# Performance work log

Measured on AMD Instinct MI355X. Metric: run time of the kernel, lower is better.

Reference implementation:

```python
import jax, jax.numpy as jnp
import numpy as np

NUM_HEADS = 16
NUM_KV_HEADS = 4
HEAD_SIZE = 128
SCALE = 1.0 / np.sqrt(128.0).astype(np.float32)
NEG_INF = -1e30


def setup_inputs() -> dict:
    key = jax.random.key(0)
    kq, kk, kv = jax.random.split(key, 3)
    B, S = 2, 2048
    query = jax.random.normal(kq, (B, NUM_HEADS, S, HEAD_SIZE), dtype=jnp.float32)
    k = jax.random.normal(kk, (B, NUM_KV_HEADS, S, HEAD_SIZE), dtype=jnp.float32)
    v = jax.random.normal(kv, (B, NUM_KV_HEADS, S, HEAD_SIZE), dtype=jnp.float32)
    return {"query": query, "key": k, "value": v}


def _attn(query, key, value):
    # query: [B, H, S, D]; key/value: [B, Hkv, S, D]; GQA with group = H // Hkv
    B, H, S, D = query.shape
    Hkv = key.shape[1]
    G = H // Hkv
    q = query.reshape(B, Hkv, G, S, D)
    # scores: [B, Hkv, G, Sq, Sk]
    scores = jnp.einsum('bkgsd,bktd->bkgst', q, key) * jnp.float32(SCALE)
    causal = jnp.tril(jnp.ones((S, S), dtype=bool))  # [Sq, Sk]
    scores = jnp.where(causal, scores, jnp.float32(NEG_INF))
    probs = jax.nn.softmax(scores, axis=-1)
    out = jnp.einsum('bkgst,bktd->bkgsd', probs, value)  # [B, Hkv, G, S, D]
    out = out.reshape(B, H, S, D)
    # transpose(1,2).reshape -> [B, S, H*D]
    return out.transpose(0, 2, 1, 3).reshape(B, S, H * D)


def reference(query, key, value):
    return _attn(query, key, value)
```

## Files before the change

kernel.cpp:

```cpp
#include <hip/hip_runtime.h>


#define S_LEN 2048
#define DH    128
#define NH    16
#define NKVH  4
#define NB    2
#define TQ    128
#define TK    64
#define NQT   (S_LEN / TQ)
#define QSCALE 0.12752749610559243f

typedef __attribute__((ext_vector_type(8))) short short8;
typedef __attribute__((ext_vector_type(4))) float f32x4;

#if __has_builtin(__builtin_amdgcn_exp2f)
#define EX2(x) __builtin_amdgcn_exp2f(x)
#else
#define EX2(x) exp2f(x)
#endif

__device__ __forceinline__ unsigned pk2(float a, float b) {
    union { float f; unsigned u; } x, y; x.f = a; y.f = b;
    return ((x.u + 0x8000u) >> 16) | ((y.u + 0x8000u) & 0xffff0000u);
}
__device__ __forceinline__ void cp16(const void* g, void* lds) {
    __builtin_amdgcn_global_load_lds(
        (const __attribute__((address_space(1))) void*)g,
        (__attribute__((address_space(3))) void*)lds, 16, 0, 0);
}

__global__ __launch_bounds__(256, 4)
void prepack(const float* __restrict__ K, const float* __restrict__ V,
             unsigned short* __restrict__ Kb, unsigned short* __restrict__ Vt) {
    if (blockIdx.y == 0) {
        const long long flat = (long long)blockIdx.x * 2048 + threadIdx.x * 8;
        const int s = (int)(flat >> 7) & (S_LEN - 1);
        const int d0 = (int)flat & 127;
        const float* p = K + flat;
        float4 x = *(const float4*)p;
        float4 y = *(const float4*)(p + 4);
        const int cs = (d0 >> 3) ^ (s & 7);
        uint4 o;
        o.x = pk2(x.x, x.y); o.y = pk2(x.z, x.w);
        o.z = pk2(y.x, y.y); o.w = pk2(y.z, y.w);
        *(uint4*)(Kb + (flat & ~127LL) + cs * 8) = o;
    } else {
        const int x = blockIdx.x;
        const int bkvh = x >> 7, sblk = (x >> 2) & 31, q = x & 3;
        const int tid = threadIdx.x;
        __shared__ unsigned Lt[64][17];
        const float* base = V + (size_t)bkvh * S_LEN * DH + (size_t)sblk * 64 * DH + q * 32;
#pragma unroll
        for (int j = 0; j < 2; ++j) {
            const int e = tid + j * 256;
            const int s = e >> 3, c4 = e & 7;
            float4 v = *(const float4*)(base + (size_t)s * DH + c4 * 4);
            Lt[s][c4 * 2]     = pk2(v.x, v.y);
            Lt[s][c4 * 2 + 1] = pk2(v.z, v.w);
        }
        __syncthreads();
        const unsigned short* lt = (const unsigned short*)&Lt[0][0];
        const int d_loc = tid >> 3, pc = tid & 7;
        const int d = q * 32 + d_loc;
        const int c_log = pc ^ (d & 7);
        unsigned short vv[8];
#pragma unroll
        for (int j = 0; j < 8; ++j) {
            const int kp = c_log * 8 + j;
            const int kv = (kp & 3) * 16 + (kp >> 2);
            vv[j] = lt[kv * 34 + d_loc];
        }
        uint4 o;
        o.x = (unsigned)vv[0] | ((unsigned)vv[1] << 16);
        o.y = (unsigned)vv[2] | ((unsigned)vv[3] << 16);
        o.z = (unsigned)vv[4] | ((unsigned)vv[5] << 16);
        o.w = (unsigned)vv[6] | ((unsigned)vv[7] << 16);
        *(uint4*)(Vt + (size_t)bkvh * S_LEN * DH + (size_t)d * S_LEN + sblk * 64 + pc * 8) = o;
    }
}

__global__ __launch_bounds__(256, 2)
void attn_fwd(const float* __restrict__ Q,
              const unsigned short* __restrict__ Kb,
              const unsigned short* __restrict__ Vtg,
              float* __restrict__ O,
              float* __restrict__ Opart,
              float* __restrict__ Lpart) {
    const int n    = blockIdx.x;
    const int g    = n & 7;
    const int b    = g >> 2;
    const int kvh  = g & 3;
    const int kk   = n >> 3;
    const int h    = kvh * 4 + (kk & 3);
    const int pr   = kk >> 2;
    const int a    = pr & 7;
    const int role = pr >> 3;
    const int sid  = ((b * NH + h) << 3) + a;

    const int tid  = threadIdx.x;
    const int w    = tid >> 6;
    const int lane = tid & 63;
    const int quad = lane >> 4;
    const int l16  = lane & 15;
    const int swz  = l16 & 7;

    int qt0, kt00, nr0, qt1; bool two_seg;
    if (role == 0) { qt0 = a;      kt00 = 0;         nr0 = 2 * a + 2;
                     qt1 = 15 - a; two_seg = true; }
    else           { qt0 = 15 - a; kt00 = 15 - 2*a;  nr0 = 17;
                     qt1 = 0;      two_seg = false; }

    __shared__ alignas(16) unsigned short Kl[2][TK][DH];
    __shared__ alignas(16) unsigned short Vl[2][DH][TK];
    __shared__ alignas(16) unsigned short Pl[TQ][64];

    const unsigned short* kb = Kb  + ((size_t)b * NKVH + kvh) * (size_t)(S_LEN * DH);
    const unsigned short* vb = Vtg + ((size_t)b * NKVH + kvh) * (size_t)(S_LEN * DH);

    auto stage = [&](int nb_, int kt) {
        const char* ks = (const char*)(kb + (size_t)kt * TK * DH);
        char* kd = (char*)&Kl[nb_][0][0] + w * 4096;
#pragma unroll
        for (int i = 0; i < 4; ++i)
            cp16(ks + w * 4096 + i * 1024 + lane * 16, kd + i * 1024);
        const char* vs = (const char*)vb + (size_t)kt * (TK * 2);
        char* vd = (char*)&Vl[nb_][0][0] + w * 4096;
#pragma unroll
        for (int i = 0; i < 4; ++i) {
            const int row = w * 32 + i * 8 + (lane >> 3);
            cp16(vs + (size_t)row * (S_LEN * 2) + (lane & 7) * 16, vd + i * 1024);
        }
    };
    auto ktof = [&](int r) { return r < nr0 ? kt00 + r : r - nr0; };

    stage(0, ktof(0));

    int qt  = qt0;
    int wq0 = qt * TQ + w * 32;
    int ntw = 2 * qt + 1 + (w >> 1);

    short8 aq[2][4];
    auto loadQ = [&]() {
#pragma unroll
        for (int sub = 0; sub < 2; ++sub) {
            const float* qp = Q + (((size_t)b * NH + h) * S_LEN + wq0 + sub * 16 + l16) * DH;
#pragma unroll
            for (int dc = 0; dc < 4; ++dc) {
                float4 xx = *(const float4*)(qp + dc * 32 + quad * 8);
                float4 yy = *(const float4*)(qp + dc * 32 + quad * 8 + 4);
                union { unsigned u[4]; short8 s; } tq;
                tq.u[0] = pk2(xx.x * QSCALE, xx.y * QSCALE);
                tq.u[1] = pk2(xx.z * QSCALE, xx.w * QSCALE);
                tq.u[2] = pk2(yy.x * QSCALE, yy.y * QSCALE);
                tq.u[3] = pk2(yy.z * QSCALE, yy.w * QSCALE);
                aq[sub][dc] = tq.s;
            }
        }
    };
    loadQ();

    f32x4 o[2][8];
    float lsum[2][4];
#pragma unroll
    for (int sub = 0; sub < 2; ++sub) {
#pragma unroll
        for (int ch = 0; ch < 8; ++ch) o[sub][ch] = (f32x4){0.f, 0.f, 0.f, 0.f};
#pragma unroll
        for (int r = 0; r < 4; ++r) lsum[sub][r] = 0.f;
    }

    __syncthreads();

    int cur = 0;
    for (int r = 0; r < 17; ++r) {
        if (r + 1 < 17) stage(cur ^ 1, ktof(r + 1));
        const int kt = ktof(r);
        if (kt < ntw) {
            const int j0 = kt * TK;
            const bool diag = (kt == ntw - 1);
            f32x4 s[2][4];
#pragma unroll
            for (int sub = 0; sub < 2; ++sub)
#pragma unroll
                for (int k4 = 0; k4 < 4; ++k4) s[sub][k4] = (f32x4){0.f, 0.f, 0.f, 0.f};
#pragma unroll
            for (int dc = 0; dc < 4; ++dc) {
#pragma unroll
                for (int k4 = 0; k4 < 4; ++k4) {
                    short8 bk = *(const short8*)&Kl[cur][k4 * 16 + l16][((dc * 4 + quad) ^ swz) * 8];
                    s[0][k4] = __builtin_amdgcn_mfma_f32_16x16x32_bf16(aq[0][dc], bk, s[0][k4], 0, 0, 0);
                    s[1][k4] = __builtin_amdgcn_mfma_f32_16x16x32_bf16(aq[1][dc], bk, s[1][k4], 0, 0, 0);
                }
            }
#pragma unroll
            for (int sub = 0; sub < 2; ++sub) {
                const int rb = wq0 + sub * 16 + quad * 4;
#pragma unroll
                for (int rr = 0; rr < 4; ++rr) {
                    float v0 = s[sub][0][rr], v1 = s[sub][1][rr];
                    float v2 = s[sub][2][rr], v3 = s[sub][3][rr];
                    if (diag) {
                        const int row = rb + rr;
                        if (j0 + l16      > row) v0 = -1e30f;
                        if (j0 + 16 + l16 > row) v1 = -1e30f;
                        if (j0 + 32 + l16 > row) v2 = -1e30f;
                        if (j0 + 48 + l16 > row) v3 = -1e30f;
                    }
                    float p0 = EX2(v0), p1 = EX2(v1), p2 = EX2(v2), p3 = EX2(v3);
                    lsum[sub][rr] += (p0 + p1) + (p2 + p3);
                    const int prow = w * 32 + sub * 16 + quad * 4 + rr;
                    const int wcol = (l16 * 8) ^ ((prow & 7) << 4);
                    *(uint2*)((char*)&Pl[0][0] + prow * 128 + wcol) =
                        make_uint2(pk2(p0, p1), pk2(p2, p3));
                }
            }
            const int rx = (l16 & 7) << 4;
#pragma unroll
            for (int kc = 0; kc < 2; ++kc) {
                const int cb = kc * 64 + quad * 16;
                short8 ap0 = *(const short8*)((const char*)&Pl[0][0] + (w * 32 + l16) * 128 + (cb ^ rx));
                short8 ap1 = *(const short8*)((const char*)&Pl[0][0] + (w * 32 + 16 + l16) * 128 + (cb ^ rx));
#pragma unroll
                for (int ch = 0; ch < 8; ++ch) {
                    short8 bv = *(const short8*)&Vl[cur][ch * 16 + l16][((kc * 4 + quad) ^ swz) * 8];
                    o[0][ch] = __builtin_amdgcn_mfma_f32_16x16x32_bf16(ap0, bv, o[0][ch], 0, 0, 0);
                    o[1][ch] = __builtin_amdgcn_mfma_f32_16x16x32_bf16(ap1, bv, o[1][ch], 0, 0, 0);
                }
            }
        }
        __syncthreads();
        cur ^= 1;
        if (two_seg && r == nr0 - 1) {
#pragma unroll
            for (int sub = 0; sub < 2; ++sub) {
#pragma unroll
                for (int rr = 0; rr < 4; ++rr) {
                    float rs = lsum[sub][rr];
                    rs += __shfl_xor(rs, 1);
                    rs += __shfl_xor(rs, 2);
                    rs += __shfl_xor(rs, 4);
                    rs += __shfl_xor(rs, 8);
                    const float invl = 1.f / rs;
                    const int row = wq0 + sub * 16 + quad * 4 + rr;
                    float* op = O + ((size_t)b * S_LEN + row) * (NH * DH) + h * DH;
#pragma unroll
                    for (int ch = 0; ch < 8; ++ch)
                        op[ch * 16 + l16] = o[sub][ch][rr] * invl;
                }
            }
            qt = qt1; wq0 = qt * TQ + w * 32; ntw = 2 * qt + 1 + (w >> 1);
            loadQ();
#pragma unroll
            for (int sub = 0; sub < 2; ++sub) {
#pragma unroll
                for (int ch = 0; ch < 8; ++ch) o[sub][ch] = (f32x4){0.f, 0.f, 0.f, 0.f};
#pragma unroll
                for (int rr = 0; rr < 4; ++rr) lsum[sub][rr] = 0.f;
            }
        }
    }

    float* lb = Lpart + (size_t)(role * 256 + sid) * 128;
#pragma unroll
    for (int sub = 0; sub < 2; ++sub) {
#pragma unroll
        for (int rr = 0; rr < 4; ++rr) {
            float rs = lsum[sub][rr];
            rs += __shfl_xor(rs, 1);
            rs += __shfl_xor(rs, 2);
            rs += __shfl_xor(rs, 4);
            rs += __shfl_xor(rs, 8);
            const int rl = w * 32 + sub * 16 + quad * 4 + rr;
            if (l16 == 0) lb[rl] = rs;
            float* op;
            if (role == 0) {
                const int row = wq0 + sub * 16 + quad * 4 + rr;
                op = O + ((size_t)b * S_LEN + row) * (NH * DH) + h * DH;
            } else {
                op = Opart + (size_t)sid * (128 * 128) + (size_t)rl * 128;
            }
#pragma unroll
            for (int ch = 0; ch < 8; ++ch)
                op[ch * 16 + l16] = o[sub][ch][rr];
        }
    }
}

__global__ __launch_bounds__(256)
void combine(const float* __restrict__ Opart, const float* __restrict__ Lpart,
             float* __restrict__ O) {
    const int blk = blockIdx.x;
    const int sid = blk >> 2;
    const int qp  = blk & 3;
    const int bh = sid >> 3, a = sid & 7;
    const int b = bh >> 4, h = bh & 15;
    const int qt = 15 - a;
    const float* o1 = Opart + (size_t)sid * (128 * 128);
    const float* l0 = Lpart + (size_t)sid * 128;
    const float* l1 = Lpart + (size_t)(256 + sid) * 128;
    const int tid = threadIdx.x;
#pragma unroll
    for (int i = 0; i < 4; ++i) {
        const int idx = qp * 1024 + i * 256 + tid;
        const int row = idx >> 5;
        const int c4  = idx & 31;
        const float inv = 1.f / (l0[row] + l1[row]);
        float* op = O + ((size_t)b * S_LEN + qt * 128 + row) * (NH * DH) + h * DH + c4 * 4;
        const float4 x = *(const float4*)op;
        const float4 y = ((const float4*)o1)[idx];
        float4 z;
        z.x = (x.x + y.x) * inv; z.y = (x.y + y.y) * inv;
        z.z = (x.z + y.z) * inv; z.w = (x.w + y.w) * inv;
        *(float4*)op = z;
    }
}

extern "C" void kernel_launch(void* const* d_in, const int* in_sizes, int n_in,
                              void* d_out, int out_size, void* d_ws, size_t ws_size,
                              hipStream_t stream) {
    const float* Q = (const float*)d_in[0];
    const float* K = (const float*)d_in[1];
    const float* V = (const float*)d_in[2];
    float* O = (float*)d_out;
    unsigned short* Kb = (unsigned short*)d_ws;
    unsigned short* Vt = Kb + (size_t)NB * NKVH * S_LEN * DH;
    float* Opart = (float*)(Vt + (size_t)NB * NKVH * S_LEN * DH);
    float* Lpart = Opart + (size_t)256 * 128 * 128;
    dim3 pgrid(NB * NKVH * (S_LEN / 16), 2);
    prepack<<<pgrid, 256, 0, stream>>>(K, V, Kb, Vt);
    attn_fwd<<<dim3(512), 256, 0, stream>>>(Q, Kb, Vt, O, Opart, Lpart);
    combine<<<dim3(1024), 256, 0, stream>>>(Opart, Lpart, O);
}
```

Baseline: 149.6 us.

## Fuse split-KV combine into attention kernel via atomic last-arriver flag

Removes the separate combine kernel. Each pair of split blocks now increments a per-segment atomic counter after writing its partials, and the second block to arrive merges both partial outputs and normalises them directly in the attention kernel. Counters are zeroed inside the prepack kernel. The change also raises wave priority with s_setprio around the MFMA loops. It saves one kernel launch and a pass over O, at the cost of fences, an atomic and a serialized tail in the last-arriving block.

```diff
diff --git a/kernel.cpp b/kernel.cpp
--- a/kernel.cpp
+++ b/kernel.cpp
@@ -32,8 +32,10 @@
 
 __global__ __launch_bounds__(256, 4)
 void prepack(const float* __restrict__ K, const float* __restrict__ V,
-             unsigned short* __restrict__ Kb, unsigned short* __restrict__ Vt) {
+             unsigned short* __restrict__ Kb, unsigned short* __restrict__ Vt,
+             unsigned* __restrict__ Flag) {
     if (blockIdx.y == 0) {
+        if (blockIdx.x == 0) Flag[threadIdx.x] = 0u;
         const long long flat = (long long)blockIdx.x * 2048 + threadIdx.x * 8;
         const int s = (int)(flat >> 7) & (S_LEN - 1);
         const int d0 = (int)flat & 127;
@@ -86,7 +88,8 @@
               const unsigned short* __restrict__ Vtg,
               float* __restrict__ O,
               float* __restrict__ Opart,
-              float* __restrict__ Lpart) {
+              float* __restrict__ Lpart,
+              unsigned* __restrict__ Flag) {
     const int n    = blockIdx.x;
     const int g    = n & 7;
     const int b    = g >> 2;
@@ -184,6 +187,7 @@
             for (int sub = 0; sub < 2; ++sub)
 #pragma unroll
                 for (int k4 = 0; k4 < 4; ++k4) s[sub][k4] = (f32x4){0.f, 0.f, 0.f, 0.f};
+            __builtin_amdgcn_s_setprio(1);
 #pragma unroll
             for (int dc = 0; dc < 4; ++dc) {
 #pragma unroll
@@ -193,6 +197,7 @@
                     s[1][k4] = __builtin_amdgcn_mfma_f32_16x16x32_bf16(aq[1][dc], bk, s[1][k4], 0, 0, 0);
                 }
             }
+            __builtin_amdgcn_s_setprio(0);
 #pragma unroll
             for (int sub = 0; sub < 2; ++sub) {
                 const int rb = wq0 + sub * 16 + quad * 4;
@@ -216,6 +221,7 @@
                 }
             }
             const int rx = (l16 & 7) << 4;
+            __builtin_amdgcn_s_setprio(1);
 #pragma unroll
             for (int kc = 0; kc < 2; ++kc) {
                 const int cb = kc * 64 + quad * 16;
@@ -228,6 +234,7 @@
                     o[1][ch] = __builtin_amdgcn_mfma_f32_16x16x32_bf16(ap1, bv, o[1][ch], 0, 0, 0);
                 }
             }
+            __builtin_amdgcn_s_setprio(0);
         }
         __syncthreads();
         cur ^= 1;
@@ -261,58 +268,65 @@
         }
     }
 
-    float* lb = Lpart + (size_t)(role * 256 + sid) * 128;
-#pragma unroll
-    for (int sub = 0; sub < 2; ++sub) {
-#pragma unroll
-        for (int rr = 0; rr < 4; ++rr) {
-            float rs = lsum[sub][rr];
-            rs += __shfl_xor(rs, 1);
-            rs += __shfl_xor(rs, 2);
-            rs += __shfl_xor(rs, 4);
-            rs += __shfl_xor(rs, 8);
-            const int rl = w * 32 + sub * 16 + quad * 4 + rr;
-            if (l16 == 0) lb[rl] = rs;
-            float* op;
-            if (role == 0) {
+    float rsv[2][4];
+    {
+        float* lb = Lpart + (size_t)(role * 256 + sid) * 128;
+#pragma unroll
+        for (int sub = 0; sub < 2; ++sub) {
+#pragma unroll
+            for (int rr = 0; rr < 4; ++rr) {
+                float rs = lsum[sub][rr];
+                rs += __shfl_xor(rs, 1);
+                rs += __shfl_xor(rs, 2);
+                rs += __shfl_xor(rs, 4);
+                rs += __shfl_xor(rs, 8);
+                rsv[sub][rr] = rs;
+                const int rl = w * 32 + sub * 16 + quad * 4 + rr;
+                if (l16 == 0) lb[rl] = rs;
+                float* op;
+                if (role == 0) {
+                    const int row = wq0 + sub * 16 + quad * 4 + rr;
+                    op = O + ((size_t)b * S_LEN + row) * (NH * DH) + h * DH;
+                } else {
+                    op = Opart + (size_t)sid * (128 * 128) + (size_t)rl * 128;
+                }
+#pragma unroll
+                for (int ch = 0; ch < 8; ++ch)
+                    op[ch * 16 + l16] = o[sub][ch][rr];
+            }
+        }
+    }
+
+    __threadfence();
+    __syncthreads();
+    int* sflag = (int*)&Kl[0][0][0];
+    if (tid == 0) *sflag = (atomicAdd(&Flag[sid], 1u) == 1u) ? 1 : 0;
+    __syncthreads();
+    if (*sflag) {
+        __threadfence();
+        const float* lo = Lpart + (size_t)((1 - role) * 256 + sid) * 128;
+        const float* opp = Opart + (size_t)sid * (128 * 128);
+#pragma unroll
+        for (int sub = 0; sub < 2; ++sub) {
+#pragma unroll
+            for (int rr = 0; rr < 4; ++rr) {
+                const int rl  = w * 32 + sub * 16 + quad * 4 + rr;
                 const int row = wq0 + sub * 16 + quad * 4 + rr;
-                op = O + ((size_t)b * S_LEN + row) * (NH * DH) + h * DH;
-            } else {
-                op = Opart + (size_t)sid * (128 * 128) + (size_t)rl * 128;
-            }
-#pragma unroll
-            for (int ch = 0; ch < 8; ++ch)
-                op[ch * 16 + l16] = o[sub][ch][rr];
-        }
-    }
-}
-
-__global__ __launch_bounds__(256)
-void combine(const float* __restrict__ Opart, const float* __restrict__ Lpart,
-             float* __restrict__ O) {
-    const int blk = blockIdx.x;
-    const int sid = blk >> 2;
-    const int qp  = blk & 3;
-    const int bh = sid >> 3, a = sid & 7;
-    const int b = bh >> 4, h = bh & 15;
-    const int qt = 15 - a;
-    const float* o1 = Opart + (size_t)sid * (128 * 128);
-    const float* l0 = Lpart + (size_t)sid * 128;
-    const float* l1 = Lpart + (size_t)(256 + sid) * 128;
-    const int tid = threadIdx.x;
-#pragma unroll
-    for (int i = 0; i < 4; ++i) {
-        const int idx = qp * 1024 + i * 256 + tid;
-        const int row = idx >> 5;
-        const int c4  = idx & 31;
-        const float inv = 1.f / (l0[row] + l1[row]);
-        float* op = O + ((size_t)b * S_LEN + qt * 128 + row) * (NH * DH) + h * DH + c4 * 4;
-        const float4 x = *(const float4*)op;
-        const float4 y = ((const float4*)o1)[idx];
-        float4 z;
-        z.x = (x.x + y.x) * inv; z.y = (x.y + y.y) * inv;
-        z.z = (x.z + y.z) * inv; z.w = (x.w + y.w) * inv;
-        *(float4*)op = z;
+                const float inv = 1.f / (rsv[sub][rr] + lo[rl]);
+                float* op = O + ((size_t)b * S_LEN + row) * (NH * DH) + h * DH;
+                if (role == 0) {
+#pragma unroll
+                    for (int ch = 0; ch < 8; ++ch)
+                        op[ch * 16 + l16] = (o[sub][ch][rr] + opp[(size_t)rl * 128 + ch * 16 + l16]) * inv;
+                } else {
+#pragma unroll
+                    for (int ch = 0; ch < 8; ++ch) {
+                        const float peer = op[ch * 16 + l16];
+                        op[ch * 16 + l16] = (o[sub][ch][rr] + peer) * inv;
+                    }
+                }
+            }
+        }
     }
 }
 
@@ -327,8 +341,8 @@
     unsigned short* Vt = Kb + (size_t)NB * NKVH * S_LEN * DH;
     float* Opart = (float*)(Vt + (size_t)NB * NKVH * S_LEN * DH);
     float* Lpart = Opart + (size_t)256 * 128 * 128;
+    unsigned* Flag = (unsigned*)(Lpart + (size_t)512 * 128);
     dim3 pgrid(NB * NKVH * (S_LEN / 16), 2);
-    prepack<<<pgrid, 256, 0, stream>>>(K, V, Kb, Vt);
-    attn_fwd<<<dim3(512), 256, 0, stream>>>(Q, Kb, Vt, O, Opart, Lpart);
-    combine<<<dim3(1024), 256, 0, stream>>>(Opart, Lpart, O);
-}
+    prepack<<<pgrid, 256, 0, stream>>>(K, V, Kb, Vt, Flag);
+    attn_fwd<<<dim3(512), 256, 0, stream>>>(Q, Kb, Vt, O, Opart, Lpart, Flag);
+}
```

Measured after the change: 248.7 us. 1.66x slower.

## Software-pipeline QK^T of next tile with softmax/PV of previous tile

Applied to the files above, without the earlier changes.

Restructures the main loop so that the QK^T MFMAs for tile r are issued in the same iteration as the exp/P-store and PV MFMAs for tile r-1, with K and V staged separately at different offsets. Scores are carried across iterations in extra registers, and segment-end output writes are deferred by one iteration. The goal is to overlap the MFMA work with the exp/LDS work and hide load latency. The cost is higher register pressure, which may reduce occupancy, plus one extra loop iteration.

```diff
diff --git a/kernel.cpp b/kernel.cpp
--- a/kernel.cpp
+++ b/kernel.cpp
@@ -118,14 +118,16 @@
     const unsigned short* kb = Kb  + ((size_t)b * NKVH + kvh) * (size_t)(S_LEN * DH);
     const unsigned short* vb = Vtg + ((size_t)b * NKVH + kvh) * (size_t)(S_LEN * DH);
 
-    auto stage = [&](int nb_, int kt) {
+    auto stageK = [&](int buf, int kt) {
         const char* ks = (const char*)(kb + (size_t)kt * TK * DH);
-        char* kd = (char*)&Kl[nb_][0][0] + w * 4096;
+        char* kd = (char*)&Kl[buf][0][0] + w * 4096;
 #pragma unroll
         for (int i = 0; i < 4; ++i)
             cp16(ks + w * 4096 + i * 1024 + lane * 16, kd + i * 1024);
+    };
+    auto stageV = [&](int buf, int kt) {
         const char* vs = (const char*)vb + (size_t)kt * (TK * 2);
-        char* vd = (char*)&Vl[nb_][0][0] + w * 4096;
+        char* vd = (char*)&Vl[buf][0][0] + w * 4096;
 #pragma unroll
         for (int i = 0; i < 4; ++i) {
             const int row = w * 32 + i * 8 + (lane >> 3);
@@ -134,7 +136,7 @@
     };
     auto ktof = [&](int r) { return r < nr0 ? kt00 + r : r - nr0; };
 
-    stage(0, ktof(0));
+    stageK(0, ktof(0));
 
     int qt  = qt0;
     int wq0 = qt * TQ + w * 32;
@@ -172,40 +174,50 @@
 
     __syncthreads();
 
-    int cur = 0;
-    for (int r = 0; r < 17; ++r) {
-        if (r + 1 < 17) stage(cur ^ 1, ktof(r + 1));
-        const int kt = ktof(r);
-        if (kt < ntw) {
-            const int j0 = kt * TK;
-            const bool diag = (kt == ntw - 1);
-            f32x4 s[2][4];
-#pragma unroll
-            for (int sub = 0; sub < 2; ++sub)
-#pragma unroll
-                for (int k4 = 0; k4 < 4; ++k4) s[sub][k4] = (f32x4){0.f, 0.f, 0.f, 0.f};
-#pragma unroll
-            for (int dc = 0; dc < 4; ++dc) {
-#pragma unroll
-                for (int k4 = 0; k4 < 4; ++k4) {
-                    short8 bk = *(const short8*)&Kl[cur][k4 * 16 + l16][((dc * 4 + quad) ^ swz) * 8];
-                    s[0][k4] = __builtin_amdgcn_mfma_f32_16x16x32_bf16(aq[0][dc], bk, s[0][k4], 0, 0, 0);
-                    s[1][k4] = __builtin_amdgcn_mfma_f32_16x16x32_bf16(aq[1][dc], bk, s[1][k4], 0, 0, 0);
+    f32x4 sP[2][4];
+    int  p_j0 = 0, p_wq0 = 0;
+    bool p_valid = false, p_diag = false, p_segend = false;
+
+    for (int r = 0; r <= 17; ++r) {
+        if (r < 17) {
+            if (r + 1 < 17) stageK((r + 1) & 1, ktof(r + 1));
+            stageV(r & 1, ktof(r));
+        }
+        f32x4 sN[2][4];
+        bool n_valid = false; int n_j0 = 0; bool n_diag = false;
+        if (r < 17) {
+            const int kt = ktof(r);
+            if (kt < ntw) {
+                n_valid = true; n_j0 = kt * TK; n_diag = (kt == ntw - 1);
+#pragma unroll
+                for (int sub = 0; sub < 2; ++sub)
+#pragma unroll
+                    for (int k4 = 0; k4 < 4; ++k4) sN[sub][k4] = (f32x4){0.f, 0.f, 0.f, 0.f};
+#pragma unroll
+                for (int dc = 0; dc < 4; ++dc) {
+#pragma unroll
+                    for (int k4 = 0; k4 < 4; ++k4) {
+                        short8 bk = *(const short8*)&Kl[r & 1][k4 * 16 + l16][((dc * 4 + quad) ^ swz) * 8];
+                        sN[0][k4] = __builtin_amdgcn_mfma_f32_16x16x32_bf16(aq[0][dc], bk, sN[0][k4], 0, 0, 0);
+                        sN[1][k4] = __builtin_amdgcn_mfma_f32_16x16x32_bf16(aq[1][dc], bk, sN[1][k4], 0, 0, 0);
+                    }
                 }
             }
+        }
+        if (p_valid) {
 #pragma unroll
             for (int sub = 0; sub < 2; ++sub) {
-                const int rb = wq0 + sub * 16 + quad * 4;
+                const int rb = p_wq0 + sub * 16 + quad * 4;
 #pragma unroll
                 for (int rr = 0; rr < 4; ++rr) {
-                    float v0 = s[sub][0][rr], v1 = s[sub][1][rr];
-                    float v2 = s[sub][2][rr], v3 = s[sub][3][rr];
-                    if (diag) {
+                    float v0 = sP[sub][0][rr], v1 = sP[sub][1][rr];
+                    float v2 = sP[sub][2][rr], v3 = sP[sub][3][rr];
+                    if (p_diag) {
                         const int row = rb + rr;
-                        if (j0 + l16      > row) v0 = -1e30f;
-                        if (j0 + 16 + l16 > row) v1 = -1e30f;
-                        if (j0 + 32 + l16 > row) v2 = -1e30f;
-                        if (j0 + 48 + l16 > row) v3 = -1e30f;
+                        if (p_j0 + l16      > row) v0 = -1e30f;
+                        if (p_j0 + 16 + l16 > row) v1 = -1e30f;
+                        if (p_j0 + 32 + l16 > row) v2 = -1e30f;
+                        if (p_j0 + 48 + l16 > row) v3 = -1e30f;
                     }
                     float p0 = EX2(v0), p1 = EX2(v1), p2 = EX2(v2), p3 = EX2(v3);
                     lsum[sub][rr] += (p0 + p1) + (p2 + p3);
@@ -216,6 +228,7 @@
                 }
             }
             const int rx = (l16 & 7) << 4;
+            const int vbuf = (r + 1) & 1;
 #pragma unroll
             for (int kc = 0; kc < 2; ++kc) {
                 const int cb = kc * 64 + quad * 16;
@@ -223,15 +236,13 @@
                 short8 ap1 = *(const short8*)((const char*)&Pl[0][0] + (w * 32 + 16 + l16) * 128 + (cb ^ rx));
 #pragma unroll
                 for (int ch = 0; ch < 8; ++ch) {
-                    short8 bv = *(const short8*)&Vl[cur][ch * 16 + l16][((kc * 4 + quad) ^ swz) * 8];
+                    short8 bv = *(const short8*)&Vl[vbuf][ch * 16 + l16][((kc * 4 + quad) ^ swz) * 8];
                     o[0][ch] = __builtin_amdgcn_mfma_f32_16x16x32_bf16(ap0, bv, o[0][ch], 0, 0, 0);
                     o[1][ch] = __builtin_amdgcn_mfma_f32_16x16x32_bf16(ap1, bv, o[1][ch], 0, 0, 0);
                 }
             }
         }
-        __syncthreads();
-        cur ^= 1;
-        if (two_seg && r == nr0 - 1) {
+        if (p_segend) {
 #pragma unroll
             for (int sub = 0; sub < 2; ++sub) {
 #pragma unroll
@@ -242,23 +253,36 @@
                     rs += __shfl_xor(rs, 4);
                     rs += __shfl_xor(rs, 8);
                     const float invl = 1.f / rs;
-                    const int row = wq0 + sub * 16 + quad * 4 + rr;
+                    const int row = qt0 * TQ + w * 32 + sub * 16 + quad * 4 + rr;
                     float* op = O + ((size_t)b * S_LEN + row) * (NH * DH) + h * DH;
 #pragma unroll
                     for (int ch = 0; ch < 8; ++ch)
                         op[ch * 16 + l16] = o[sub][ch][rr] * invl;
                 }
             }
+#pragma unroll
+            for (int sub = 0; sub < 2; ++sub) {
+#pragma unroll
+                for (int ch = 0; ch < 8; ++ch) o[sub][ch] = (f32x4){0.f, 0.f, 0.f, 0.f};
+#pragma unroll
+                for (int rr = 0; rr < 4; ++rr) lsum[sub][rr] = 0.f;
+            }
+            p_segend = false;
+        }
+        p_valid = n_valid;
+        if (n_valid) {
+#pragma unroll
+            for (int sub = 0; sub < 2; ++sub)
+#pragma unroll
+                for (int k4 = 0; k4 < 4; ++k4) sP[sub][k4] = sN[sub][k4];
+            p_j0 = n_j0; p_diag = n_diag; p_wq0 = wq0;
+        }
+        if (two_seg && r == nr0 - 1) {
+            p_segend = true;
             qt = qt1; wq0 = qt * TQ + w * 32; ntw = 2 * qt + 1 + (w >> 1);
             loadQ();
-#pragma unroll
-            for (int sub = 0; sub < 2; ++sub) {
-#pragma unroll
-                for (int ch = 0; ch < 8; ++ch) o[sub][ch] = (f32x4){0.f, 0.f, 0.f, 0.f};
-#pragma unroll
-                for (int rr = 0; rr < 4; ++rr) lsum[sub][rr] = 0.f;
-            }
-        }
+        }
+        __syncthreads();
     }
 
     float* lb = Lpart + (size_t)(role * 256 + sid) * 128;
```

After: 164.0 us. +9.6%, slower.

## Split attention block across 8 waves with 16 query rows each

Applied to the files above, without the earlier changes.

Doubles the attention block from 4 to 8 waves, so each wave handles 16 query rows instead of 32. K/V staging is split across the extra waves. Per-wave register arrays (Q fragments, scores, output accumulators) shrink by half, and launch bounds rise to 512 threads with 4 blocks per CU to raise occupancy and latency hiding. In exchange each K/V fragment read from LDS now feeds only one MFMA instead of two, which doubles LDS read traffic per FLOP and adds more waves to each barrier.

```diff
diff --git a/kernel.cpp b/kernel.cpp
--- a/kernel.cpp
+++ b/kernel.cpp
@@ -80,7 +80,7 @@
     }
 }
 
-__global__ __launch_bounds__(256, 2)
+__global__ __launch_bounds__(512, 4)
 void attn_fwd(const float* __restrict__ Q,
               const unsigned short* __restrict__ Kb,
               const unsigned short* __restrict__ Vtg,
@@ -118,18 +118,21 @@
     const unsigned short* kb = Kb  + ((size_t)b * NKVH + kvh) * (size_t)(S_LEN * DH);
     const unsigned short* vb = Vtg + ((size_t)b * NKVH + kvh) * (size_t)(S_LEN * DH);
 
-    auto stage = [&](int nb_, int kt) {
+    auto stage = [&](int buf, int kt) {
         const char* ks = (const char*)(kb + (size_t)kt * TK * DH);
-        char* kd = (char*)&Kl[nb_][0][0] + w * 4096;
-#pragma unroll
-        for (int i = 0; i < 4; ++i)
-            cp16(ks + w * 4096 + i * 1024 + lane * 16, kd + i * 1024);
+        char* kd = (char*)&Kl[buf][0][0];
+#pragma unroll
+        for (int i = 0; i < 2; ++i) {
+            const int off = w * 2048 + i * 1024;
+            cp16(ks + off + lane * 16, kd + off);
+        }
         const char* vs = (const char*)vb + (size_t)kt * (TK * 2);
-        char* vd = (char*)&Vl[nb_][0][0] + w * 4096;
-#pragma unroll
-        for (int i = 0; i < 4; ++i) {
-            const int row = w * 32 + i * 8 + (lane >> 3);
-            cp16(vs + (size_t)row * (S_LEN * 2) + (lane & 7) * 16, vd + i * 1024);
+        char* vd = (char*)&Vl[buf][0][0];
+#pragma unroll
+        for (int i = 0; i < 2; ++i) {
+            const int off = w * 2048 + i * 1024;
+            const int row = w * 16 + i * 8 + (lane >> 3);
+            cp16(vs + (size_t)row * (S_LEN * 2) + (lane & 7) * 16, vd + off);
         }
     };
     auto ktof = [&](int r) { return r < nr0 ? kt00 + r : r - nr0; };
@@ -137,38 +140,32 @@
     stage(0, ktof(0));
 
     int qt  = qt0;
-    int wq0 = qt * TQ + w * 32;
-    int ntw = 2 * qt + 1 + (w >> 1);
-
-    short8 aq[2][4];
+    int wq0 = qt * TQ + w * 16;
+    int ntw = 2 * qt + 1 + (w >> 2);
+
+    short8 aq[4];
     auto loadQ = [&]() {
-#pragma unroll
-        for (int sub = 0; sub < 2; ++sub) {
-            const float* qp = Q + (((size_t)b * NH + h) * S_LEN + wq0 + sub * 16 + l16) * DH;
-#pragma unroll
-            for (int dc = 0; dc < 4; ++dc) {
-                float4 xx = *(const float4*)(qp + dc * 32 + quad * 8);
-                float4 yy = *(const float4*)(qp + dc * 32 + quad * 8 + 4);
-                union { unsigned u[4]; short8 s; } tq;
-                tq.u[0] = pk2(xx.x * QSCALE, xx.y * QSCALE);
-                tq.u[1] = pk2(xx.z * QSCALE, xx.w * QSCALE);
-                tq.u[2] = pk2(yy.x * QSCALE, yy.y * QSCALE);
-                tq.u[3] = pk2(yy.z * QSCALE, yy.w * QSCALE);
-                aq[sub][dc] = tq.s;
-            }
+        const float* qp = Q + (((size_t)b * NH + h) * S_LEN + wq0 + l16) * DH;
+#pragma unroll
+        for (int dc = 0; dc < 4; ++dc) {
+            float4 xx = *(const float4*)(qp + dc * 32 + quad * 8);
+            float4 yy = *(const float4*)(qp + dc * 32 + quad * 8 + 4);
+            union { unsigned u[4]; short8 s; } tq;
+            tq.u[0] = pk2(xx.x * QSCALE, xx.y * QSCALE);
+            tq.u[1] = pk2(xx.z * QSCALE, xx.w * QSCALE);
+            tq.u[2] = pk2(yy.x * QSCALE, yy.y * QSCALE);
+            tq.u[3] = pk2(yy.z * QSCALE, yy.w * QSCALE);
+            aq[dc] = tq.s;
         }
     };
     loadQ();
 
-    f32x4 o[2][8];
-    float lsum[2][4];
-#pragma unroll
-    for (int sub = 0; sub < 2; ++sub) {
-#pragma unroll
-        for (int ch = 0; ch < 8; ++ch) o[sub][ch] = (f32x4){0.f, 0.f, 0.f, 0.f};
-#pragma unroll
-        for (int r = 0; r < 4; ++r) lsum[sub][r] = 0.f;
-    }
+    f32x4 o[8];
+    float lsum[4];
+#pragma unroll
+    for (int ch = 0; ch < 8; ++ch) o[ch] = (f32x4){0.f, 0.f, 0.f, 0.f};
+#pragma unroll
+    for (int r = 0; r < 4; ++r) lsum[r] = 0.f;
 
     __syncthreads();
 
@@ -179,27 +176,23 @@
         if (kt < ntw) {
             const int j0 = kt * TK;
             const bool diag = (kt == ntw - 1);
-            f32x4 s[2][4];
-#pragma unroll
-            for (int sub = 0; sub < 2; ++sub)
-#pragma unroll
-                for (int k4 = 0; k4 < 4; ++k4) s[sub][k4] = (f32x4){0.f, 0.f, 0.f, 0.f};
+            f32x4 s[4];
+#pragma unroll
+            for (int k4 = 0; k4 < 4; ++k4) s[k4] = (f32x4){0.f, 0.f, 0.f, 0.f};
 #pragma unroll
             for (int dc = 0; dc < 4; ++dc) {
 #pragma unroll
                 for (int k4 = 0; k4 < 4; ++k4) {
                     short8 bk = *(const short8*)&Kl[cur][k4 * 16 + l16][((dc * 4 + quad) ^ swz) * 8];
-                    s[0][k4] = __builtin_amdgcn_mfma_f32_16x16x32_bf16(aq[0][dc], bk, s[0][k4], 0, 0, 0);
-                    s[1][k4] = __builtin_amdgcn_mfma_f32_16x16x32_bf16(aq[1][dc], bk, s[1][k4], 0, 0, 0);
+                    s[k4] = __builtin_amdgcn_mfma_f32_16x16x32_bf16(aq[dc], bk, s[k4], 0, 0, 0);
                 }
             }
-#pragma unroll
-            for (int sub = 0; sub < 2; ++sub) {
-                const int rb = wq0 + sub * 16 + quad * 4;
+            {
+                const int rb = wq0 + quad * 4;
 #pragma unroll
                 for (int rr = 0; rr < 4; ++rr) {
-                    float v0 = s[sub][0][rr], v1 = s[sub][1][rr];
-                    float v2 = s[sub][2][rr], v3 = s[sub][3][rr];
+                    float v0 = s[0][rr], v1 = s[1][rr];
+                    float v2 = s[2][rr], v3 = s[3][rr];
                     if (diag) {
                         const int row = rb + rr;
                         if (j0 + l16      > row) v0 = -1e30f;
@@ -208,8 +201,8 @@
                         if (j0 + 48 + l16 > row) v3 = -1e30f;
                     }
                     float p0 = EX2(v0), p1 = EX2(v1), p2 = EX2(v2), p3 = EX2(v3);
-                    lsum[sub][rr] += (p0 + p1) + (p2 + p3);
-                    const int prow = w * 32 + sub * 16 + quad * 4 + rr;
+                    lsum[rr] += (p0 + p1) + (p2 + p3);
+                    const int prow = w * 16 + quad * 4 + rr;
                     const int wcol = (l16 * 8) ^ ((prow & 7) << 4);
                     *(uint2*)((char*)&Pl[0][0] + prow * 128 + wcol) =
                         make_uint2(pk2(p0, p1), pk2(p2, p3));
@@ -219,13 +212,11 @@
 #pragma unroll
             for (int kc = 0; kc < 2; ++kc) {
                 const int cb = kc * 64 + quad * 16;
-                short8 ap0 = *(const short8*)((const char*)&Pl[0][0] + (w * 32 + l16) * 128 + (cb ^ rx));
-                short8 ap1 = *(const short8*)((const char*)&Pl[0][0] + (w * 32 + 16 + l16) * 128 + (cb ^ rx));
+                short8 ap = *(const short8*)((const char*)&Pl[0][0] + (w * 16 + l16) * 128 + (cb ^ rx));
 #pragma unroll
                 for (int ch = 0; ch < 8; ++ch) {
                     short8 bv = *(const short8*)&Vl[cur][ch * 16 + l16][((kc * 4 + quad) ^ swz) * 8];
-                    o[0][ch] = __builtin_amdgcn_mfma_f32_16x16x32_bf16(ap0, bv, o[0][ch], 0, 0, 0);
-                    o[1][ch] = __builtin_amdgcn_mfma_f32_16x16x32_bf16(ap1, bv, o[1][ch], 0, 0, 0);
+                    o[ch] = __builtin_amdgcn_mfma_f32_16x16x32_bf16(ap, bv, o[ch], 0, 0, 0);
                 }
             }
         }
@@ -233,57 +224,48 @@
         cur ^= 1;
         if (two_seg && r == nr0 - 1) {
 #pragma unroll
-            for (int sub = 0; sub < 2; ++sub) {
-#pragma unroll
-                for (int rr = 0; rr < 4; ++rr) {
-                    float rs = lsum[sub][rr];
-                    rs += __shfl_xor(rs, 1);
-                    rs += __shfl_xor(rs, 2);
-                    rs += __shfl_xor(rs, 4);
-                    rs += __shfl_xor(rs, 8);
-                    const float invl = 1.f / rs;
-                    const int row = wq0 + sub * 16 + quad * 4 + rr;
-                    float* op = O + ((size_t)b * S_LEN + row) * (NH * DH) + h * DH;
-#pragma unroll
-                    for (int ch = 0; ch < 8; ++ch)
-                        op[ch * 16 + l16] = o[sub][ch][rr] * invl;
-                }
+            for (int rr = 0; rr < 4; ++rr) {
+                float rs = lsum[rr];
+                rs += __shfl_xor(rs, 1);
+                rs += __shfl_xor(rs, 2);
+                rs += __shfl_xor(rs, 4);
+                rs += __shfl_xor(rs, 8);
+                const float invl = 1.f / rs;
+                const int row = wq0 + quad * 4 + rr;
+                float* op = O + ((size_t)b * S_LEN + row) * (NH * DH) + h * DH;
+#pragma unroll
+                for (int ch = 0; ch < 8; ++ch)
+                    op[ch * 16 + l16] = o[ch][rr] * invl;
             }
-            qt = qt1; wq0 = qt * TQ + w * 32; ntw = 2 * qt + 1 + (w >> 1);
+            qt = qt1; wq0 = qt * TQ + w * 16; ntw = 2 * qt + 1 + (w >> 2);
             loadQ();
 #pragma unroll
-            for (int sub = 0; sub < 2; ++sub) {
-#pragma unroll
-                for (int ch = 0; ch < 8; ++ch) o[sub][ch] = (f32x4){0.f, 0.f, 0.f, 0.f};
-#pragma unroll
-                for (int rr = 0; rr < 4; ++rr) lsum[sub][rr] = 0.f;
-            }
+            for (int ch = 0; ch < 8; ++ch) o[ch] = (f32x4){0.f, 0.f, 0.f, 0.f};
+#pragma unroll
+            for (int rr = 0; rr < 4; ++rr) lsum[rr] = 0.f;
         }
     }
 
     float* lb = Lpart + (size_t)(role * 256 + sid) * 128;
 #pragma unroll
-    for (int sub = 0; sub < 2; ++sub) {
-#pragma unroll
-        for (int rr = 0; rr < 4; ++rr) {
-            float rs = lsum[sub][rr];
-            rs += __shfl_xor(rs, 1);
-            rs += __shfl_xor(rs, 2);
-            rs += __shfl_xor(rs, 4);
-            rs += __shfl_xor(rs, 8);
-            const int rl = w * 32 + sub * 16 + quad * 4 + rr;
-            if (l16 == 0) lb[rl] = rs;
-            float* op;
-            if (role == 0) {
-                const int row = wq0 + sub * 16 + quad * 4 + rr;
-                op = O + ((size_t)b * S_LEN + row) * (NH * DH) + h * DH;
-            } else {
-                op = Opart + (size_t)sid * (128 * 128) + (size_t)rl * 128;
-            }
-#pragma unroll
-            for (int ch = 0; ch < 8; ++ch)
-                op[ch * 16 + l16] = o[sub][ch][rr];
-        }
+    for (int rr = 0; rr < 4; ++rr) {
+        float rs = lsum[rr];
+        rs += __shfl_xor(rs, 1);
+        rs += __shfl_xor(rs, 2);
+        rs += __shfl_xor(rs, 4);
+        rs += __shfl_xor(rs, 8);
+        const int rl = w * 16 + quad * 4 + rr;
+        if (l16 == 0) lb[rl] = rs;
+        float* op;
+        if (role == 0) {
+            const int row = wq0 + quad * 4 + rr;
+            op = O + ((size_t)b * S_LEN + row) * (NH * DH) + h * DH;
+        } else {
+            op = Opart + (size_t)sid * (128 * 128) + (size_t)rl * 128;
+        }
+#pragma unroll
+        for (int ch = 0; ch < 8; ++ch)
+            op[ch * 16 + l16] = o[ch][rr];
     }
 }
 
@@ -329,6 +311,6 @@
     float* Lpart = Opart + (size_t)256 * 128 * 128;
     dim3 pgrid(NB * NKVH * (S_LEN / 16), 2);
     prepack<<<pgrid, 256, 0, stream>>>(K, V, Kb, Vt);
-    attn_fwd<<<dim3(512), 256, 0, stream>>>(Q, Kb, Vt, O, Opart, Lpart);
+    attn_fwd<<<dim3(512), 512, 0, stream>>>(Q, Kb, Vt, O, Opart, Lpart);
     combine<<<dim3(1024), 256, 0, stream>>>(Opart, Lpart, O);
 }
```

Result: no change. 148.1 us (-1.0%).
